# Optimization experiments

Hardware: AMD Instinct MI355X
Metric: run time of the kernel (lower is better)

Reference implementation:

```python
import jax, jax.numpy as jnp
import numpy as np

BRANCH = 4
DEPTH = 5                      # complete 4-ary tree: leaves = 4**5 = 1024
N_NODES = (BRANCH ** (DEPTH + 1) - 1) // (BRANCH - 1)   # 1365
FIRST_LEAF = (BRANCH ** DEPTH - 1) // (BRANCH - 1)       # 341
N_LEAVES = BRANCH ** DEPTH     # 1024
F, C = 512, 64                 # layer_shape
MIN_DISTANCE = 1e-07


def _build_tree():
    parent = np.zeros(N_NODES, dtype=np.int32)
    for i in range(1, N_NODES):
        parent[i] = (i - 1) // BRANCH
    # ancestor-or-self matrix: anc[i, j] = 1 iff j is on path root->i
    anc = np.zeros((N_NODES, N_NODES), dtype=np.int32)
    for i in range(N_NODES):
        j = i
        while True:
            anc[i, j] = 1
            if j == 0:
                break
            j = parent[j]
    leaf_ids = np.arange(FIRST_LEAF, N_NODES, dtype=np.int32)  # [1024]
    return parent, anc, leaf_ids


def setup_inputs() -> dict:
    key = jax.random.key(0)
    k_x, k_d, k_h = jax.random.split(key, 3)
    parent, anc, leaf_ids = _build_tree()
    x = jax.random.normal(k_x, (N_LEAVES, F), dtype=jnp.float32)
    # per-node AdditionLayer weights (the learned deltas)
    deltas = jax.random.normal(k_d, (N_NODES, F, C), dtype=jnp.float32) * 0.05
    heights = jax.random.uniform(k_h, (N_NODES,), dtype=jnp.float32)
    return {
        "x": x,
        "deltas": deltas,
        "heights": heights,
        "anc": jnp.asarray(anc),
        "parent": jnp.asarray(parent),
        "leaf_ids": jnp.asarray(leaf_ids),
    }


def reference(x, deltas, heights, anc, parent, leaf_ids):
    n = deltas.shape[0]
    # --- regularization (delta_tensor) ---
    # root: parent is None -> squared difference vs input (zeros): sum(delta_0^2)
    reg_root = jnp.sum(jnp.square(deltas[0]))
    # non-root: sum(|curr - input|) / max(|h - h_parent|, min_distance)
    dist = jnp.maximum(jnp.abs(heights - heights[parent]), MIN_DISTANCE)  # [N]
    l1 = jnp.sum(jnp.abs(deltas), axis=(1, 2))                            # [N]
    reg_rest = jnp.sum(l1[1:] / dist[1:])
    delta_tensor = jnp.reshape(reg_root + reg_rest, (1,))
    # --- path-sum of deltas: each node's effective weights ---
    anc_f = anc.astype(deltas.dtype)                    # [N, N]
    cum_flat = anc_f @ deltas.reshape(n, -1)            # [N, F*C]
    w_leaf = cum_flat[leaf_ids].reshape(-1, F, C)       # [L, F, C]
    logits = jnp.einsum("bf,bfc->bc", x, w_leaf)        # [L, C]
    out = jax.nn.softmax(logits, axis=-1)
    return out, delta_tensor
```

## Files before the change

kernel.cpp:

```cpp
#include <hip/hip_runtime.h>

#define FDIM 512
#define CDIM 64
#define NLEAF 1024
#define MAT (FDIM * CDIM)
#define OUT_LOGITS (NLEAF * CDIM)
#define WS_REG (NLEAF * CDIM)

__device__ __forceinline__ float abs4(const float4 v) {
    return fabsf(v.x) + fabsf(v.y) + fabsf(v.z) + fabsf(v.w);
}
__device__ __forceinline__ float sq4(const float4 v) {
    return v.x * v.x + v.y * v.y + v.z * v.z + v.w * v.w;
}

template<int MODE>
__device__ __forceinline__ void stream2(const float* __restrict__ dbase,
                                        const float4 xr[2][4],
                                        float4* __restrict__ acc,
                                        float& rsum, float s)
{
#pragma unroll
    for (int h = 0; h < 4; ++h) {
        const float* q = dbase + (size_t)(4 * h) * CDIM;
        const float4 d0 = *(const float4*)(q);
        const float4 d1 = *(const float4*)(q + CDIM);
        const float4 d2 = *(const float4*)(q + 2 * CDIM);
        const float4 d3 = *(const float4*)(q + 3 * CDIM);
        if (MODE == 1) rsum = fmaf(abs4(d0) + abs4(d1) + abs4(d2) + abs4(d3), s, rsum);
        if (MODE == 2) rsum += sq4(d0) + sq4(d1) + sq4(d2) + sq4(d3);
#pragma unroll
        for (int r = 0; r < 2; ++r) {
            const float4 xv = xr[r][h];
            acc[r].x += xv.x * d0.x + xv.y * d1.x + xv.z * d2.x + xv.w * d3.x;
            acc[r].y += xv.x * d0.y + xv.y * d1.y + xv.z * d2.y + xv.w * d3.y;
            acc[r].z += xv.x * d0.z + xv.y * d1.z + xv.z * d2.z + xv.w * d3.z;
            acc[r].w += xv.x * d0.w + xv.y * d1.w + xv.z * d2.w + xv.w * d3.w;
        }
    }
}

template<int R>
__device__ __forceinline__ void stream1(const float* __restrict__ dbase,
                                        const float4 xr[2][4],
                                        float4* __restrict__ acc,
                                        float& rsum, float s)
{
#pragma unroll
    for (int h = 0; h < 4; ++h) {
        const float* q = dbase + (size_t)(4 * h) * CDIM;
        const float4 d0 = *(const float4*)(q);
        const float4 d1 = *(const float4*)(q + CDIM);
        const float4 d2 = *(const float4*)(q + 2 * CDIM);
        const float4 d3 = *(const float4*)(q + 3 * CDIM);
        rsum = fmaf(abs4(d0) + abs4(d1) + abs4(d2) + abs4(d3), s, rsum);
        const float4 xv = xr[R][h];
        acc[R].x += xv.x * d0.x + xv.y * d1.x + xv.z * d2.x + xv.w * d3.x;
        acc[R].y += xv.x * d0.y + xv.y * d1.y + xv.z * d2.y + xv.w * d3.y;
        acc[R].z += xv.x * d0.z + xv.y * d1.z + xv.z * d2.z + xv.w * d3.z;
        acc[R].w += xv.x * d0.w + xv.y * d1.w + xv.z * d2.w + xv.w * d3.w;
    }
}

__global__ __launch_bounds__(256, 2) void k_fused(const float* __restrict__ x,
                                                  const float* __restrict__ deltas,
                                                  const float* __restrict__ heights,
                                                  float* __restrict__ ws)
{
    __shared__ float red[4 * 64];
    __shared__ float rr[4];

    const int tid = threadIdx.x;
    const int bid = blockIdx.x;
    const int k  = bid & 7;
    const int t  = bid >> 3;
    const int p  = (k << 6) | (t >> 1);
    const int ch = t & 1;
    const int l0 = 2 * p;
    const int fg = tid >> 3;
    const int cq = tid & 7;
    const int c0 = ch * 32 + cq * 4;

    float4 xr[2][4];
#pragma unroll
    for (int r = 0; r < 2; ++r)
#pragma unroll
        for (int j = 0; j < 4; ++j)
            xr[r][j] = *(const float4*)(x + (size_t)(l0 + r) * FDIM + fg * 16 + 4 * j);

    float4 acc[2];
    acc[0] = make_float4(0.f, 0.f, 0.f, 0.f);
    acc[1] = make_float4(0.f, 0.f, 0.f, 0.f);
    float rsum = 0.f;
    const size_t toff = (size_t)(fg * 16) * CDIM + c0;

#pragma unroll
    for (int d = 0; d < 5; ++d) {
        const int shift = 2 * (5 - d);
        const int start = ((1 << (2 * d)) - 1) / 3;
        const int node  = start + (l0 >> shift);
        const float* dbase = deltas + (size_t)node * MAT + toff;
        const bool doReg = (l0 & ((1 << shift) - 1)) == 0;
        if (d == 0) {
            if (doReg) stream2<2>(dbase, xr, acc, rsum, 1.f);
            else       stream2<0>(dbase, xr, acc, rsum, 0.f);
        } else {
            if (doReg) {
                const int par = (node - 1) >> 2;
                const float s = 1.f / fmaxf(fabsf(heights[node] - heights[par]), 1e-7f);
                stream2<1>(dbase, xr, acc, rsum, s);
            } else {
                stream2<0>(dbase, xr, acc, rsum, 0.f);
            }
        }
    }

    {
        const int n5 = 341 + l0;
        const float hp = heights[85 + (l0 >> 2)];
        const float sA = 1.f / fmaxf(fabsf(heights[n5]     - hp), 1e-7f);
        stream1<0>(deltas + (size_t)n5 * MAT + toff, xr, acc, rsum, sA);
        __builtin_amdgcn_sched_barrier(0);
        const float sB = 1.f / fmaxf(fabsf(heights[n5 + 1] - hp), 1e-7f);
        stream1<1>(deltas + (size_t)(n5 + 1) * MAT + toff, xr, acc, rsum, sB);
    }

#pragma unroll
    for (int r = 0; r < 2; ++r) {
        acc[r].x += __shfl_xor(acc[r].x, 8, 64); acc[r].x += __shfl_xor(acc[r].x, 16, 64); acc[r].x += __shfl_xor(acc[r].x, 32, 64);
        acc[r].y += __shfl_xor(acc[r].y, 8, 64); acc[r].y += __shfl_xor(acc[r].y, 16, 64); acc[r].y += __shfl_xor(acc[r].y, 32, 64);
        acc[r].z += __shfl_xor(acc[r].z, 8, 64); acc[r].z += __shfl_xor(acc[r].z, 16, 64); acc[r].z += __shfl_xor(acc[r].z, 32, 64);
        acc[r].w += __shfl_xor(acc[r].w, 8, 64); acc[r].w += __shfl_xor(acc[r].w, 16, 64); acc[r].w += __shfl_xor(acc[r].w, 32, 64);
    }

    const int w = tid >> 6, lane = tid & 63;
    if (lane < 8) {
#pragma unroll
        for (int r = 0; r < 2; ++r)
            *(float4*)(red + w * 64 + r * 32 + cq * 4) = acc[r];
    }

#pragma unroll
    for (int off = 1; off < 64; off <<= 1) rsum += __shfl_xor(rsum, off, 64);
    if (lane == 0) rr[w] = rsum;
    __syncthreads();

    if (tid < 64) {
        const int r = tid >> 5, cc = tid & 31;
        const float v = red[0 * 64 + r * 32 + cc] + red[1 * 64 + r * 32 + cc]
                      + red[2 * 64 + r * 32 + cc] + red[3 * 64 + r * 32 + cc];
        ws[(size_t)(l0 + r) * CDIM + ch * 32 + cc] = v;
    }
    if (tid == 64)
        ws[WS_REG + bid] = rr[0] + rr[1] + rr[2] + rr[3];
}

__global__ __launch_bounds__(256) void k_finish(const float* __restrict__ ws,
                                                float* __restrict__ out)
{
    const int l = blockIdx.x * 4 + (threadIdx.x >> 6);
    const int c = threadIdx.x & 63;
    const float v = ws[(size_t)l * CDIM + c];
    float m = v;
#pragma unroll
    for (int off = 32; off > 0; off >>= 1) m = fmaxf(m, __shfl_xor(m, off, 64));
    const float e = expf(v - m);
    float s = e;
#pragma unroll
    for (int off = 32; off > 0; off >>= 1) s += __shfl_xor(s, off, 64);
    out[(size_t)l * CDIM + c] = e / s;
}

__global__ __launch_bounds__(256) void k_regsum(const float* __restrict__ ws,
                                                float* __restrict__ out)
{
    __shared__ float r[4];
    const int tid = threadIdx.x;
    const float* p = ws + WS_REG;
    float v = p[tid] + p[256 + tid] + p[512 + tid] + p[768 + tid];
#pragma unroll
    for (int off = 1; off < 64; off <<= 1) v += __shfl_xor(v, off, 64);
    if ((tid & 63) == 0) r[tid >> 6] = v;
    __syncthreads();
    if (tid == 0) out[OUT_LOGITS] = r[0] + r[1] + r[2] + r[3];
}

extern "C" void kernel_launch(void* const* d_in, const int* in_sizes, int n_in,
                              void* d_out, int out_size, void* d_ws, size_t ws_size,
                              hipStream_t stream)
{
    const float* x       = (const float*)d_in[0];
    const float* deltas  = (const float*)d_in[1];
    const float* heights = (const float*)d_in[2];
    float* out = (float*)d_out;
    float* ws  = (float*)d_ws;

    k_fused<<<NLEAF, 256, 0, stream>>>(x, deltas, heights, ws);
    k_finish<<<256, 256, 0, stream>>>(ws, out);
    k_regsum<<<1, 256, 0, stream>>>(ws, out);
}
```

Baseline: 39.24 us.

## Process four sibling leaves per block to share ancestor delta loads

Each block now handles the four leaves that share a parent instead of two, with 512 threads that each cover 8 features rather than 16. Every ancestor delta slice is loaded once and reused across four leaves, which cuts the redundant reads of internal-node weights. The grid is halved to 512 blocks and the shared-memory reduction, the per-block regularisation partials and the final regsum are adjusted to match. The trade-off is more accumulator registers per thread, fewer blocks, and a larger cross-warp reduction.

```diff
diff --git a/kernel.cpp b/kernel.cpp
--- a/kernel.cpp
+++ b/kernel.cpp
@@ -15,13 +15,13 @@
 }
 
 template<int MODE>
-__device__ __forceinline__ void stream2(const float* __restrict__ dbase,
-                                        const float4 xr[2][4],
+__device__ __forceinline__ void stream4(const float* __restrict__ dbase,
+                                        const float4 xr[4][2],
                                         float4* __restrict__ acc,
                                         float& rsum, float s)
 {
 #pragma unroll
-    for (int h = 0; h < 4; ++h) {
+    for (int h = 0; h < 2; ++h) {
         const float* q = dbase + (size_t)(4 * h) * CDIM;
         const float4 d0 = *(const float4*)(q);
         const float4 d1 = *(const float4*)(q + CDIM);
@@ -30,7 +30,7 @@
         if (MODE == 1) rsum = fmaf(abs4(d0) + abs4(d1) + abs4(d2) + abs4(d3), s, rsum);
         if (MODE == 2) rsum += sq4(d0) + sq4(d1) + sq4(d2) + sq4(d3);
 #pragma unroll
-        for (int r = 0; r < 2; ++r) {
+        for (int r = 0; r < 4; ++r) {
             const float4 xv = xr[r][h];
             acc[r].x += xv.x * d0.x + xv.y * d1.x + xv.z * d2.x + xv.w * d3.x;
             acc[r].y += xv.x * d0.y + xv.y * d1.y + xv.z * d2.y + xv.w * d3.y;
@@ -41,13 +41,13 @@
 }
 
 template<int R>
-__device__ __forceinline__ void stream1(const float* __restrict__ dbase,
-                                        const float4 xr[2][4],
-                                        float4* __restrict__ acc,
-                                        float& rsum, float s)
-{
-#pragma unroll
-    for (int h = 0; h < 4; ++h) {
+__device__ __forceinline__ void leaf1(const float* __restrict__ dbase,
+                                      const float4 xr[4][2],
+                                      float4* __restrict__ acc,
+                                      float& rsum, float s)
+{
+#pragma unroll
+    for (int h = 0; h < 2; ++h) {
         const float* q = dbase + (size_t)(4 * h) * CDIM;
         const float4 d0 = *(const float4*)(q);
         const float4 d1 = *(const float4*)(q + CDIM);
@@ -62,37 +62,38 @@
     }
 }
 
-__global__ __launch_bounds__(256, 2) void k_fused(const float* __restrict__ x,
+__global__ __launch_bounds__(512, 2) void k_fused(const float* __restrict__ x,
                                                   const float* __restrict__ deltas,
                                                   const float* __restrict__ heights,
                                                   float* __restrict__ ws)
 {
-    __shared__ float red[4 * 64];
-    __shared__ float rr[4];
+    __shared__ float red[8 * 132];
+    __shared__ float rr[8];
 
     const int tid = threadIdx.x;
     const int bid = blockIdx.x;
     const int k  = bid & 7;
     const int t  = bid >> 3;
-    const int p  = (k << 6) | (t >> 1);
+    const int q  = (k << 5) | (t >> 1);
     const int ch = t & 1;
-    const int l0 = 2 * p;
+    const int l0 = 4 * q;
     const int fg = tid >> 3;
     const int cq = tid & 7;
+    const int f0 = fg * 8;
     const int c0 = ch * 32 + cq * 4;
 
-    float4 xr[2][4];
-#pragma unroll
-    for (int r = 0; r < 2; ++r)
-#pragma unroll
-        for (int j = 0; j < 4; ++j)
-            xr[r][j] = *(const float4*)(x + (size_t)(l0 + r) * FDIM + fg * 16 + 4 * j);
-
-    float4 acc[2];
-    acc[0] = make_float4(0.f, 0.f, 0.f, 0.f);
-    acc[1] = make_float4(0.f, 0.f, 0.f, 0.f);
+    float4 xr[4][2];
+#pragma unroll
+    for (int r = 0; r < 4; ++r)
+#pragma unroll
+        for (int j = 0; j < 2; ++j)
+            xr[r][j] = *(const float4*)(x + (size_t)(l0 + r) * FDIM + f0 + 4 * j);
+
+    float4 acc[4];
+#pragma unroll
+    for (int r = 0; r < 4; ++r) acc[r] = make_float4(0.f, 0.f, 0.f, 0.f);
     float rsum = 0.f;
-    const size_t toff = (size_t)(fg * 16) * CDIM + c0;
+    const size_t toff = (size_t)f0 * CDIM + c0;
 
 #pragma unroll
     for (int d = 0; d < 5; ++d) {
@@ -102,31 +103,37 @@
         const float* dbase = deltas + (size_t)node * MAT + toff;
         const bool doReg = (l0 & ((1 << shift) - 1)) == 0;
         if (d == 0) {
-            if (doReg) stream2<2>(dbase, xr, acc, rsum, 1.f);
-            else       stream2<0>(dbase, xr, acc, rsum, 0.f);
+            if (doReg) stream4<2>(dbase, xr, acc, rsum, 1.f);
+            else       stream4<0>(dbase, xr, acc, rsum, 0.f);
         } else {
             if (doReg) {
                 const int par = (node - 1) >> 2;
                 const float s = 1.f / fmaxf(fabsf(heights[node] - heights[par]), 1e-7f);
-                stream2<1>(dbase, xr, acc, rsum, s);
+                stream4<1>(dbase, xr, acc, rsum, s);
             } else {
-                stream2<0>(dbase, xr, acc, rsum, 0.f);
+                stream4<0>(dbase, xr, acc, rsum, 0.f);
             }
         }
     }
 
     {
         const int n5 = 341 + l0;
-        const float hp = heights[85 + (l0 >> 2)];
-        const float sA = 1.f / fmaxf(fabsf(heights[n5]     - hp), 1e-7f);
-        stream1<0>(deltas + (size_t)n5 * MAT + toff, xr, acc, rsum, sA);
+        const float hp = heights[85 + q];
+        const float s0 = 1.f / fmaxf(fabsf(heights[n5 + 0] - hp), 1e-7f);
+        leaf1<0>(deltas + (size_t)(n5 + 0) * MAT + toff, xr, acc, rsum, s0);
         __builtin_amdgcn_sched_barrier(0);
-        const float sB = 1.f / fmaxf(fabsf(heights[n5 + 1] - hp), 1e-7f);
-        stream1<1>(deltas + (size_t)(n5 + 1) * MAT + toff, xr, acc, rsum, sB);
-    }
-
-#pragma unroll
-    for (int r = 0; r < 2; ++r) {
+        const float s1 = 1.f / fmaxf(fabsf(heights[n5 + 1] - hp), 1e-7f);
+        leaf1<1>(deltas + (size_t)(n5 + 1) * MAT + toff, xr, acc, rsum, s1);
+        __builtin_amdgcn_sched_barrier(0);
+        const float s2 = 1.f / fmaxf(fabsf(heights[n5 + 2] - hp), 1e-7f);
+        leaf1<2>(deltas + (size_t)(n5 + 2) * MAT + toff, xr, acc, rsum, s2);
+        __builtin_amdgcn_sched_barrier(0);
+        const float s3 = 1.f / fmaxf(fabsf(heights[n5 + 3] - hp), 1e-7f);
+        leaf1<3>(deltas + (size_t)(n5 + 3) * MAT + toff, xr, acc, rsum, s3);
+    }
+
+#pragma unroll
+    for (int r = 0; r < 4; ++r) {
         acc[r].x += __shfl_xor(acc[r].x, 8, 64); acc[r].x += __shfl_xor(acc[r].x, 16, 64); acc[r].x += __shfl_xor(acc[r].x, 32, 64);
         acc[r].y += __shfl_xor(acc[r].y, 8, 64); acc[r].y += __shfl_xor(acc[r].y, 16, 64); acc[r].y += __shfl_xor(acc[r].y, 32, 64);
         acc[r].z += __shfl_xor(acc[r].z, 8, 64); acc[r].z += __shfl_xor(acc[r].z, 16, 64); acc[r].z += __shfl_xor(acc[r].z, 32, 64);
@@ -136,8 +143,8 @@
     const int w = tid >> 6, lane = tid & 63;
     if (lane < 8) {
 #pragma unroll
-        for (int r = 0; r < 2; ++r)
-            *(float4*)(red + w * 64 + r * 32 + cq * 4) = acc[r];
+        for (int r = 0; r < 4; ++r)
+            *(float4*)(red + w * 132 + r * 32 + cq * 4) = acc[r];
     }
 
 #pragma unroll
@@ -145,14 +152,20 @@
     if (lane == 0) rr[w] = rsum;
     __syncthreads();
 
-    if (tid < 64) {
+    if (tid < 128) {
         const int r = tid >> 5, cc = tid & 31;
-        const float v = red[0 * 64 + r * 32 + cc] + red[1 * 64 + r * 32 + cc]
-                      + red[2 * 64 + r * 32 + cc] + red[3 * 64 + r * 32 + cc];
+        float v = 0.f;
+#pragma unroll
+        for (int w2 = 0; w2 < 8; ++w2)
+            v += red[w2 * 132 + r * 32 + cc];
         ws[(size_t)(l0 + r) * CDIM + ch * 32 + cc] = v;
     }
-    if (tid == 64)
-        ws[WS_REG + bid] = rr[0] + rr[1] + rr[2] + rr[3];
+    if (tid == 128) {
+        float v = 0.f;
+#pragma unroll
+        for (int w2 = 0; w2 < 8; ++w2) v += rr[w2];
+        ws[WS_REG + bid] = v;
+    }
 }
 
 __global__ __launch_bounds__(256) void k_finish(const float* __restrict__ ws,
@@ -177,7 +190,7 @@
     __shared__ float r[4];
     const int tid = threadIdx.x;
     const float* p = ws + WS_REG;
-    float v = p[tid] + p[256 + tid] + p[512 + tid] + p[768 + tid];
+    float v = p[tid] + p[256 + tid];
 #pragma unroll
     for (int off = 1; off < 64; off <<= 1) v += __shfl_xor(v, off, 64);
     if ((tid & 63) == 0) r[tid >> 6] = v;
@@ -195,7 +208,7 @@
     float* out = (float*)d_out;
     float* ws  = (float*)d_ws;
 
-    k_fused<<<NLEAF, 256, 0, stream>>>(x, deltas, heights, ws);
+    k_fused<<<512, 512, 0, stream>>>(x, deltas, heights, ws);
     k_finish<<<256, 256, 0, stream>>>(ws, out);
     k_regsum<<<1, 256, 0, stream>>>(ws, out);
 }
```

Result: no change. 39.83 us (+1.5%).

## Fuse softmax into main kernel with full-row 512-thread blocks

Applied to the files above, without the earlier changes.

Each block now handles both leaf rows across all 64 output columns using 512 threads, instead of splitting the columns over two 256-thread blocks. Because a block then holds complete logit rows, it applies the softmax itself and writes the final output directly, and the separate k_finish launch and its workspace round-trip are removed. The regularization partials drop to 512 per-block entries, and k_regsum is adjusted to sum them. In exchange, launch_bounds(512,2) may constrain registers, and the grid has half as many blocks.

```diff
diff --git a/kernel.cpp b/kernel.cpp
--- a/kernel.cpp
+++ b/kernel.cpp
@@ -5,7 +5,6 @@
 #define NLEAF 1024
 #define MAT (FDIM * CDIM)
 #define OUT_LOGITS (NLEAF * CDIM)
-#define WS_REG (NLEAF * CDIM)
 
 __device__ __forceinline__ float abs4(const float4 v) {
     return fabsf(v.x) + fabsf(v.y) + fabsf(v.z) + fabsf(v.w);
@@ -62,24 +61,23 @@
     }
 }
 
-__global__ __launch_bounds__(256, 2) void k_fused(const float* __restrict__ x,
+__global__ __launch_bounds__(512, 2) void k_fused(const float* __restrict__ x,
                                                   const float* __restrict__ deltas,
                                                   const float* __restrict__ heights,
+                                                  float* __restrict__ out,
                                                   float* __restrict__ ws)
 {
-    __shared__ float red[4 * 64];
-    __shared__ float rr[4];
+    __shared__ float red[8 * 132];
+    __shared__ float rr[8];
 
     const int tid = threadIdx.x;
     const int bid = blockIdx.x;
     const int k  = bid & 7;
     const int t  = bid >> 3;
-    const int p  = (k << 6) | (t >> 1);
-    const int ch = t & 1;
+    const int p  = (k << 6) | t;
     const int l0 = 2 * p;
-    const int fg = tid >> 3;
-    const int cq = tid & 7;
-    const int c0 = ch * 32 + cq * 4;
+    const int fg = tid >> 4;
+    const int cq = tid & 15;
 
     float4 xr[2][4];
 #pragma unroll
@@ -92,7 +90,7 @@
     acc[0] = make_float4(0.f, 0.f, 0.f, 0.f);
     acc[1] = make_float4(0.f, 0.f, 0.f, 0.f);
     float rsum = 0.f;
-    const size_t toff = (size_t)(fg * 16) * CDIM + c0;
+    const size_t toff = (size_t)(fg * 16) * CDIM + cq * 4;
 
 #pragma unroll
     for (int d = 0; d < 5; ++d) {
@@ -127,17 +125,17 @@
 
 #pragma unroll
     for (int r = 0; r < 2; ++r) {
-        acc[r].x += __shfl_xor(acc[r].x, 8, 64); acc[r].x += __shfl_xor(acc[r].x, 16, 64); acc[r].x += __shfl_xor(acc[r].x, 32, 64);
-        acc[r].y += __shfl_xor(acc[r].y, 8, 64); acc[r].y += __shfl_xor(acc[r].y, 16, 64); acc[r].y += __shfl_xor(acc[r].y, 32, 64);
-        acc[r].z += __shfl_xor(acc[r].z, 8, 64); acc[r].z += __shfl_xor(acc[r].z, 16, 64); acc[r].z += __shfl_xor(acc[r].z, 32, 64);
-        acc[r].w += __shfl_xor(acc[r].w, 8, 64); acc[r].w += __shfl_xor(acc[r].w, 16, 64); acc[r].w += __shfl_xor(acc[r].w, 32, 64);
+        acc[r].x += __shfl_xor(acc[r].x, 16, 64);  acc[r].x += __shfl_xor(acc[r].x, 32, 64);
+        acc[r].y += __shfl_xor(acc[r].y, 16, 64);  acc[r].y += __shfl_xor(acc[r].y, 32, 64);
+        acc[r].z += __shfl_xor(acc[r].z, 16, 64);  acc[r].z += __shfl_xor(acc[r].z, 32, 64);
+        acc[r].w += __shfl_xor(acc[r].w, 16, 64);  acc[r].w += __shfl_xor(acc[r].w, 32, 64);
     }
 
     const int w = tid >> 6, lane = tid & 63;
-    if (lane < 8) {
+    if (lane < 16) {
 #pragma unroll
         for (int r = 0; r < 2; ++r)
-            *(float4*)(red + w * 64 + r * 32 + cq * 4) = acc[r];
+            *(float4*)(red + w * 132 + r * 64 + cq * 4) = acc[r];
     }
 
 #pragma unroll
@@ -145,30 +143,26 @@
     if (lane == 0) rr[w] = rsum;
     __syncthreads();
 
-    if (tid < 64) {
-        const int r = tid >> 5, cc = tid & 31;
-        const float v = red[0 * 64 + r * 32 + cc] + red[1 * 64 + r * 32 + cc]
-                      + red[2 * 64 + r * 32 + cc] + red[3 * 64 + r * 32 + cc];
-        ws[(size_t)(l0 + r) * CDIM + ch * 32 + cc] = v;
+    if (tid < 128) {
+        const int r = tid >> 6;
+        const int c = tid & 63;
+        float v = 0.f;
+#pragma unroll
+        for (int w2 = 0; w2 < 8; ++w2) v += red[w2 * 132 + r * 64 + c];
+        float m = v;
+#pragma unroll
+        for (int off = 32; off > 0; off >>= 1) m = fmaxf(m, __shfl_xor(m, off, 64));
+        const float e = expf(v - m);
+        float s2 = e;
+#pragma unroll
+        for (int off = 32; off > 0; off >>= 1) s2 += __shfl_xor(s2, off, 64);
+        out[(size_t)(l0 + r) * CDIM + c] = e / s2;
+    } else if (tid == 128) {
+        float v = 0.f;
+#pragma unroll
+        for (int w2 = 0; w2 < 8; ++w2) v += rr[w2];
+        ws[bid] = v;
     }
-    if (tid == 64)
-        ws[WS_REG + bid] = rr[0] + rr[1] + rr[2] + rr[3];
-}
-
-__global__ __launch_bounds__(256) void k_finish(const float* __restrict__ ws,
-                                                float* __restrict__ out)
-{
-    const int l = blockIdx.x * 4 + (threadIdx.x >> 6);
-    const int c = threadIdx.x & 63;
-    const float v = ws[(size_t)l * CDIM + c];
-    float m = v;
-#pragma unroll
-    for (int off = 32; off > 0; off >>= 1) m = fmaxf(m, __shfl_xor(m, off, 64));
-    const float e = expf(v - m);
-    float s = e;
-#pragma unroll
-    for (int off = 32; off > 0; off >>= 1) s += __shfl_xor(s, off, 64);
-    out[(size_t)l * CDIM + c] = e / s;
 }
 
 __global__ __launch_bounds__(256) void k_regsum(const float* __restrict__ ws,
@@ -176,8 +170,7 @@
 {
     __shared__ float r[4];
     const int tid = threadIdx.x;
-    const float* p = ws + WS_REG;
-    float v = p[tid] + p[256 + tid] + p[512 + tid] + p[768 + tid];
+    float v = ws[tid] + ws[256 + tid];
 #pragma unroll
     for (int off = 1; off < 64; off <<= 1) v += __shfl_xor(v, off, 64);
     if ((tid & 63) == 0) r[tid >> 6] = v;
@@ -195,7 +188,6 @@
     float* out = (float*)d_out;
     float* ws  = (float*)d_ws;
 
-    k_fused<<<NLEAF, 256, 0, stream>>>(x, deltas, heights, ws);
-    k_finish<<<256, 256, 0, stream>>>(ws, out);
+    k_fused<<<512, 512, 0, stream>>>(x, deltas, heights, out, ws);
     k_regsum<<<1, 256, 0, stream>>>(ws, out);
 }
```

New measurement: 41.17 us. 4.9% more time.
